# Performance work log

Hardware: AMD Instinct MI355X
Metric: run time of the kernel (lower is better)

The kernel has to match this reference:

```python
import jax, jax.numpy as jnp
import numpy as np

N = 50000
E = 800000
IN_C, OUT_C, K = 96, 16, 3
L1 = IN_C - (IN_C - OUT_C) // 3            # 70
L2 = IN_C - (2 * (IN_C - OUT_C)) // 3      # 43


def setup_inputs() -> dict:
    key = jax.random.key(0)
    ks = jax.random.split(key, 12)
    x = jax.random.normal(ks[0], (N, IN_C), dtype=jnp.float32)
    edge_index = jax.random.randint(ks[1], (2, E), 0, N, dtype=jnp.int64)

    def glorot(k, shape):
        fan_in, fan_out = shape[-2], shape[-1]
        lim = jnp.sqrt(6.0 / (fan_in + fan_out)).astype(jnp.float32)
        return jax.random.uniform(k, shape, jnp.float32, -lim, lim)

    W1 = glorot(ks[2], (K + 1, IN_C, L1)); b1 = jnp.zeros((L1,), jnp.float32)
    W2 = glorot(ks[3], (K + 1, L1, L2));   b2 = jnp.zeros((L2,), jnp.float32)
    Wmu = glorot(ks[4], (L2, OUT_C));      bmu = jnp.zeros((OUT_C,), jnp.float32)
    Wls = glorot(ks[5], (L2, OUT_C));      bls = jnp.zeros((OUT_C,), jnp.float32)
    return {"x": x, "edge_index": edge_index, "W1": W1, "b1": b1,
            "W2": W2, "b2": b2, "Wmu": Wmu, "bmu": bmu, "Wls": Wls, "bls": bls}


def _norm_no_self_loops(row, col):
    # gcn_norm, add_self_loops=False (TAGConv default)
    deg = jax.ops.segment_sum(jnp.ones((E,), jnp.float32), col, num_segments=N)
    dis = jnp.where(deg > 0, jax.lax.rsqrt(jnp.maximum(deg, 1.0)), 0.0)
    return dis[row] * dis[col]  # [E]


def _tag_conv(x, W, b, row, col, norm):
    # out = sum_k A_hat^k x W_k + b
    out = x @ W[0]
    h = x
    for k in range(1, K + 1):
        h = jax.ops.segment_sum(norm[:, None] * h[row], col, num_segments=N)
        out = out + h @ W[k]
    return out + b


def _gcn_conv(x, W, b, row, col, dis2):
    # gcn_norm with self-loops: dis2 = (deg+1)^{-1/2}
    y = x @ W
    norm = dis2[row] * dis2[col]
    agg = jax.ops.segment_sum(norm[:, None] * y[row], col, num_segments=N)
    return agg + (dis2 * dis2)[:, None] * y + b  # self-loop term + bias


def reference(x, edge_index, W1, b1, W2, b2, Wmu, bmu, Wls, bls):
    row, col = edge_index[0], edge_index[1]
    norm = _norm_no_self_loops(row, col)
    h = jax.nn.relu(_tag_conv(x, W1, b1, row, col, norm))
    h = jax.nn.relu(_tag_conv(h, W2, b2, row, col, norm))
    deg = jax.ops.segment_sum(jnp.ones((E,), jnp.float32), col, num_segments=N)
    dis2 = jax.lax.rsqrt(deg + 1.0)  # self-loops added -> deg+1 > 0
    mu = _gcn_conv(h, Wmu, bmu, row, col, dis2)
    logstd = _gcn_conv(h, Wls, bls, row, col, dis2)
    return mu, logstd
```

## Files before the change

### kernel.cpp

```cpp
#include <hip/hip_runtime.h>
#include <hip/hip_fp16.h>

static constexpr int NN  = 50000;
static constexpr int EE  = 800000;
static constexpr int CIN = 96;
static constexpr int L1C = 70, S1 = 72;
static constexpr int L2C = 43, S2P = 48;

static constexpr int IMG1U = CIN * S1 / 2;
static constexpr int IMG2U = S1 * S2P / 2;
static constexpr int IMGHU = S2P * 32 / 2;
static constexpr int NU1 = 4 * IMG1U;
static constexpr int NU2 = 4 * IMG2U;
static constexpr int TUW = NU1 + NU2 + IMGHU;
static constexpr int NBF = S1 + S2P;

static constexpr int NSLICE = 8;
static constexpr int SLICEN = NN / NSLICE;

__device__ __forceinline__ float bf_lo(unsigned int u) {
    return __uint_as_float(u << 16);
}
__device__ __forceinline__ float bf_hi(unsigned int u) {
    return __uint_as_float(u & 0xffff0000u);
}
__device__ __forceinline__ unsigned int bf_rne_bits(float f) {
    unsigned int u = __float_as_uint(f);
    return u + 0x7fffu + ((u >> 16) & 1u);
}
__device__ __forceinline__ unsigned int pack_bf(float a, float b) {
    return (bf_rne_bits(a) >> 16) | (bf_rne_bits(b) & 0xffff0000u);
}
__device__ __forceinline__ float4 unpack_bf4(uint2 q) {
    return make_float4(bf_lo(q.x), bf_hi(q.x), bf_lo(q.y), bf_hi(q.y));
}
__device__ __forceinline__ void unpack_bf8(uint4 q, float* f) {
    f[0] = bf_lo(q.x); f[1] = bf_hi(q.x); f[2] = bf_lo(q.y); f[3] = bf_hi(q.y);
    f[4] = bf_lo(q.z); f[5] = bf_hi(q.z); f[6] = bf_lo(q.w); f[7] = bf_hi(q.w);
}

__device__ __forceinline__ int rec_src(unsigned int p) { return (int)(p & 0xffffu); }
__device__ __forceinline__ float rec_w(unsigned int p) {
    return __half2float(__ushort_as_half((unsigned short)(p >> 16)));
}


__global__ void init_kernel(const float* __restrict__ W1, const float* __restrict__ b1,
                            const float* __restrict__ W2, const float* __restrict__ b2,
                            const float* __restrict__ Wmu, const float* __restrict__ Wls,
                            unsigned int* __restrict__ wB, float* __restrict__ bB,
                            int* __restrict__ deg) {
    int i = blockIdx.x * blockDim.x + threadIdx.x;
    if (i < NN) deg[i] = 0;
    if (i < TUW) {
        float v0 = 0.f, v1 = 0.f;
        if (i < NU1) {
            int img = i / IMG1U, r = i - img * IMG1U;
            int k = r / (S1 / 2), c0 = (r - k * (S1 / 2)) * 2;
            const float* Wi = W1 + (size_t)img * CIN * L1C + (size_t)k * L1C;
            if (c0 < L1C) v0 = Wi[c0];
            if (c0 + 1 < L1C) v1 = Wi[c0 + 1];
        } else if (i < NU1 + NU2) {
            int j = i - NU1;
            int img = j / IMG2U, r = j - img * IMG2U;
            int k = r / (S2P / 2), c0 = (r - k * (S2P / 2)) * 2;
            if (k < L1C) {
                const float* Wi = W2 + (size_t)img * L1C * L2C + (size_t)k * L2C;
                if (c0 < L2C) v0 = Wi[c0];
                if (c0 + 1 < L2C) v1 = Wi[c0 + 1];
            }
        } else {
            int j = i - NU1 - NU2;
            int k = j / 16, c0 = (j - k * 16) * 2;
            if (k < L2C) {
                v0 = (c0 < 16) ? Wmu[k * 16 + c0] : Wls[k * 16 + (c0 - 16)];
                int c1 = c0 + 1;
                v1 = (c1 < 16) ? Wmu[k * 16 + c1] : Wls[k * 16 + (c1 - 16)];
            }
        }
        wB[i] = pack_bf(v0, v1);
    } else if (i < TUW + NBF) {
        int j = i - TUW;
        float v = 0.f;
        if (j < S1) { if (j < L1C) v = b1[j]; }
        else { int k = j - S1; if (k < L2C) v = b2[k]; }
        bB[j] = v;
    }
}

__global__ void hist_kernel(const int* __restrict__ row, const int* __restrict__ col,
                            int* __restrict__ deg, unsigned int* __restrict__ rr, int E) {
    int e = blockIdx.x * blockDim.x + threadIdx.x;
    if (e < E) {
        int c = col[e];
        int rk = atomicAdd(&deg[c], 1);
        rr[e] = ((unsigned int)rk << 16) | (unsigned int)row[e];
    }
}

static constexpr int SB = 256;

__global__ void reduce_kernel(const int* __restrict__ deg, int* __restrict__ bsum, int n) {
    __shared__ int sd[SB];
    int i = blockIdx.x * SB + threadIdx.x;
    sd[threadIdx.x] = (i < n) ? deg[i] : 0;
    __syncthreads();
    for (int s = SB / 2; s > 0; s >>= 1) {
        if (threadIdx.x < s) sd[threadIdx.x] += sd[threadIdx.x + s];
        __syncthreads();
    }
    if (threadIdx.x == 0) bsum[blockIdx.x] = sd[0];
}

__global__ void block_scan_kernel(const int* __restrict__ deg, const int* __restrict__ bsum,
                                  int* __restrict__ off,
                                  float* __restrict__ dis, float* __restrict__ dis2,
                                  int n, int nb) {
    __shared__ int sd[SB];
    __shared__ int bofs;
    int t = threadIdx.x;
    sd[t] = (t < nb && t < (int)blockIdx.x) ? bsum[t] : 0;
    __syncthreads();
    for (int s = SB / 2; s > 0; s >>= 1) {
        if (t < s) sd[t] += sd[t + s];
        __syncthreads();
    }
    if (t == 0) bofs = sd[0];
    __syncthreads();
    int i = blockIdx.x * SB + t;
    int v = (i < n) ? deg[i] : 0;
    sd[t] = v;
    __syncthreads();
    for (int s = 1; s < SB; s <<= 1) {
        int tv = (t >= s) ? sd[t - s] : 0;
        __syncthreads();
        sd[t] += tv;
        __syncthreads();
    }
    if (i < n) {
        int e = bofs + sd[t] - v;
        off[i] = e;
        dis[i]  = (v > 0) ? rsqrtf((float)v) : 0.0f;
        dis2[i] = rsqrtf((float)v + 1.0f);
        if (i == n - 1) off[n] = e + v;
    }
}

__global__ void fill_kernel(const int* __restrict__ col, const unsigned int* __restrict__ rr,
                            const float* __restrict__ dis, const int* __restrict__ off,
                            unsigned int* __restrict__ eTag, int E) {
    int s = blockIdx.x & (NSLICE - 1);
    int nlo = s * SLICEN, nhi = nlo + SLICEN;
    int stride = (gridDim.x >> 3) * blockDim.x;
    for (int e = (blockIdx.x >> 3) * blockDim.x + threadIdx.x; e < E; e += stride) {
        int c = col[e];
        if (c >= nlo && c < nhi) {
            unsigned int u = rr[e];
            int r = (int)(u & 0xffffu);
            int pos = off[c] + (int)(u >> 16);
            unsigned short h = __half_as_ushort(__float2half(dis[r] * dis[c]));
            eTag[pos] = (unsigned int)r | ((unsigned int)h << 16);
        }
    }
}

template <int C, bool HASADD, bool RELU>
__global__ void aggw_kernel(const unsigned short* __restrict__ in, const unsigned short* addv,
                            unsigned short* out, const int* __restrict__ off,
                            const unsigned int* __restrict__ ep, int n) {
    constexpr int TPN = C / 8;
    int t = blockIdx.x * blockDim.x + threadIdx.x;
    if (t >= n * TPN) return;
    int node = t / TPN;
    int cc = (t - node * TPN) * 8;
    int beg = off[node], end = off[node + 1];
    float a0[8], a1[8];
    #pragma unroll
    for (int j = 0; j < 8; ++j) { a0[j] = 0.f; a1[j] = 0.f; }
    int e = beg;
    for (; e + 4 <= end; e += 4) {
        unsigned int p0 = ep[e], p1 = ep[e + 1], p2 = ep[e + 2], p3 = ep[e + 3];
        float w0 = rec_w(p0), w1 = rec_w(p1), w2 = rec_w(p2), w3 = rec_w(p3);
        uint4 q0 = *reinterpret_cast<const uint4*>(in + (size_t)rec_src(p0) * C + cc);
        uint4 q1 = *reinterpret_cast<const uint4*>(in + (size_t)rec_src(p1) * C + cc);
        uint4 q2 = *reinterpret_cast<const uint4*>(in + (size_t)rec_src(p2) * C + cc);
        uint4 q3 = *reinterpret_cast<const uint4*>(in + (size_t)rec_src(p3) * C + cc);
        float f[8];
        unpack_bf8(q0, f);
        #pragma unroll
        for (int j = 0; j < 8; ++j) a0[j] += w0 * f[j];
        unpack_bf8(q1, f);
        #pragma unroll
        for (int j = 0; j < 8; ++j) a1[j] += w1 * f[j];
        unpack_bf8(q2, f);
        #pragma unroll
        for (int j = 0; j < 8; ++j) a0[j] += w2 * f[j];
        unpack_bf8(q3, f);
        #pragma unroll
        for (int j = 0; j < 8; ++j) a1[j] += w3 * f[j];
    }
    for (; e < end; ++e) {
        unsigned int p = ep[e];
        float w = rec_w(p);
        uint4 q = *reinterpret_cast<const uint4*>(in + (size_t)rec_src(p) * C + cc);
        float f[8];
        unpack_bf8(q, f);
        #pragma unroll
        for (int j = 0; j < 8; ++j) a0[j] += w * f[j];
    }
    float r[8];
    #pragma unroll
    for (int j = 0; j < 8; ++j) r[j] = a0[j] + a1[j];
    if constexpr (HASADD) {
        uint4 qa = *reinterpret_cast<const uint4*>(addv + (size_t)node * C + cc);
        float f[8];
        unpack_bf8(qa, f);
        #pragma unroll
        for (int j = 0; j < 8; ++j) r[j] += f[j];
    }
    if constexpr (RELU) {
        #pragma unroll
        for (int j = 0; j < 8; ++j) r[j] = fmaxf(r[j], 0.f);
    }
    uint4 o;
    o.x = pack_bf(r[0], r[1]); o.y = pack_bf(r[2], r[3]);
    o.z = pack_bf(r[4], r[5]); o.w = pack_bf(r[6], r[7]);
    *reinterpret_cast<uint4*>(out + (size_t)node * C + cc) = o;
}

__global__ void agg_gcn_final_kernel(const unsigned short* __restrict__ yh,
                                     const int* __restrict__ off,
                                     const unsigned int* __restrict__ ep,
                                     const float* __restrict__ dis2,
                                     const float* __restrict__ bmu,
                                     const float* __restrict__ bls,
                                     float* __restrict__ outp, int n) {
    int t = blockIdx.x * blockDim.x + threadIdx.x;
    if (t >= n * 4) return;
    int node = t >> 2;
    int cc = (t & 3) * 8;
    int beg = off[node], end = off[node + 1];
    float a0[8], a1[8];
    #pragma unroll
    for (int j = 0; j < 8; ++j) { a0[j] = 0.f; a1[j] = 0.f; }
    int e = beg;
    for (; e + 2 <= end; e += 2) {
        int s0 = rec_src(ep[e]), s1 = rec_src(ep[e + 1]);
        float w0 = dis2[s0], w1 = dis2[s1];
        uint4 q0 = *reinterpret_cast<const uint4*>(yh + (size_t)s0 * 32 + cc);
        uint4 q1 = *reinterpret_cast<const uint4*>(yh + (size_t)s1 * 32 + cc);
        float f[8];
        unpack_bf8(q0, f);
        #pragma unroll
        for (int j = 0; j < 8; ++j) a0[j] += w0 * f[j];
        unpack_bf8(q1, f);
        #pragma unroll
        for (int j = 0; j < 8; ++j) a1[j] += w1 * f[j];
    }
    for (; e < end; ++e) {
        int s = rec_src(ep[e]);
        float w = dis2[s];
        uint4 q = *reinterpret_cast<const uint4*>(yh + (size_t)s * 32 + cc);
        float f[8];
        unpack_bf8(q, f);
        #pragma unroll
        for (int j = 0; j < 8; ++j) a0[j] += w * f[j];
    }
    float d = dis2[node];
    uint4 qy = *reinterpret_cast<const uint4*>(yh + (size_t)node * 32 + cc);
    float yv[8];
    unpack_bf8(qy, yv);
    const float* bp = (cc < 16) ? (bmu + cc) : (bls + (cc - 16));
    float r[8];
    #pragma unroll
    for (int j = 0; j < 8; ++j)
        r[j] = d * (a0[j] + a1[j]) + d * d * yv[j] + bp[j];
    size_t o = (cc < 16) ? ((size_t)node * 16 + cc)
                         : ((size_t)n * 16 + (size_t)node * 16 + (cc - 16));
    *reinterpret_cast<float4*>(outp + o) = make_float4(r[0], r[1], r[2], r[3]);
    *reinterpret_cast<float4*>(outp + o + 4) = make_float4(r[4], r[5], r[6], r[7]);
}

__device__ __forceinline__ void fma4(float4& a, float s, const float4& w) {
    a.x += s * w.x; a.y += s * w.y; a.z += s * w.z; a.w += s * w.w;
}

template <int KR, int PC, int NW, bool XBF, bool OBF, bool BIAS>
__global__ void mml_kernel(const void* __restrict__ Xv, const unsigned int* __restrict__ Wp,
                           const float* __restrict__ bp,
                           void* __restrict__ o0v, void* __restrict__ o1v,
                           void* __restrict__ o2v, void* __restrict__ o3v, int n) {
    constexpr int CP4 = PC / 4;
    constexpr int PCU = PC / 2;
    constexpr int WU = NW * KR * PCU;
    __shared__ __align__(16) unsigned int Wl[WU];
    __shared__ __align__(16) float bl[PC];
    {
        const uint4* s4 = reinterpret_cast<const uint4*>(Wp);
        uint4* d4 = reinterpret_cast<uint4*>(Wl);
        for (int i = threadIdx.x; i < WU / 4; i += blockDim.x) d4[i] = s4[i];
        if constexpr (BIAS)
            for (int i = threadIdx.x; i < PC; i += blockDim.x) bl[i] = bp[i];
    }
    __syncthreads();
    int idx = blockIdx.x * blockDim.x + threadIdx.x;
    if (idx >= (n >> 1) * CP4) return;
    int pair = idx / CP4;
    int c0 = (idx - pair * CP4) * 4;
    int n0 = pair * 2;
    const float* xaf = (const float*)Xv + (size_t)n0 * KR;
    const float* xbf = xaf + KR;
    const unsigned short* xah = (const unsigned short*)Xv + (size_t)n0 * KR;
    const unsigned short* xbh = xah + KR;
    const unsigned int* wc = Wl + (c0 >> 1);
    float4 acc[2][NW];
    #pragma unroll
    for (int w = 0; w < NW; ++w) {
        acc[0][w] = make_float4(0.f, 0.f, 0.f, 0.f);
        acc[1][w] = acc[0][w];
    }
    if constexpr (BIAS) {
        acc[0][0] = *reinterpret_cast<const float4*>(&bl[c0]);
        acc[1][0] = acc[0][0];
    }
    #pragma unroll 2
    for (int k4 = 0; k4 < KR / 4; ++k4) {
        float4 va, vb;
        if constexpr (XBF) {
            va = unpack_bf4(*reinterpret_cast<const uint2*>(xah + k4 * 4));
            vb = unpack_bf4(*reinterpret_cast<const uint2*>(xbh + k4 * 4));
        } else {
            va = *reinterpret_cast<const float4*>(xaf + k4 * 4);
            vb = *reinterpret_cast<const float4*>(xbf + k4 * 4);
        }
        #pragma unroll
        for (int j = 0; j < 4; ++j) {
            int k = k4 * 4 + j;
            float sa = (&va.x)[j];
            float sb = (&vb.x)[j];
            #pragma unroll
            for (int w = 0; w < NW; ++w) {
                uint2 q = *reinterpret_cast<const uint2*>(wc + (size_t)(w * KR + k) * PCU);
                float4 wv = unpack_bf4(q);
                fma4(acc[0][w], sa, wv);
                fma4(acc[1][w], sb, wv);
            }
        }
    }
    void* outs[4] = {o0v, o1v, o2v, o3v};
    #pragma unroll
    for (int w = 0; w < NW; ++w) {
        if constexpr (OBF) {
            unsigned short* o = (unsigned short*)outs[w] + (size_t)n0 * PC + c0;
            *reinterpret_cast<uint2*>(o) =
                make_uint2(pack_bf(acc[0][w].x, acc[0][w].y), pack_bf(acc[0][w].z, acc[0][w].w));
            *reinterpret_cast<uint2*>(o + PC) =
                make_uint2(pack_bf(acc[1][w].x, acc[1][w].y), pack_bf(acc[1][w].z, acc[1][w].w));
        } else {
            float* o = (float*)outs[w] + (size_t)n0 * PC + c0;
            *reinterpret_cast<float4*>(o) = acc[0][w];
            *reinterpret_cast<float4*>(o + PC) = acc[1][w];
        }
    }
}


extern "C" void kernel_launch(void* const* d_in, const int* in_sizes, int n_in,
                              void* d_out, int out_size, void* d_ws, size_t ws_size,
                              hipStream_t stream) {
    const float* x   = (const float*)d_in[0];
    const int*   ei  = (const int*)d_in[1];
    const float* W1  = (const float*)d_in[2];
    const float* b1  = (const float*)d_in[3];
    const float* W2  = (const float*)d_in[4];
    const float* b2  = (const float*)d_in[5];
    const float* Wmu = (const float*)d_in[6];
    const float* bmu = (const float*)d_in[7];
    const float* Wls = (const float*)d_in[8];
    const float* bls = (const float*)d_in[9];
    float* out = (float*)d_out;

    const int N = NN, E = EE;
    const int* row = ei;
    const int* col = ei + E;

    char* p = (char*)d_ws;
    auto alloc = [&](size_t bytes) -> char* {
        char* r = p;
        p += (bytes + 255) & ~(size_t)255;
        return r;
    };
    int*   deg    = (int*)alloc((size_t)N * 4);
    int*   off    = (int*)alloc((size_t)(N + 1) * 4);
    int*   bsum   = (int*)alloc((size_t)256 * 4);
    float* dis    = (float*)alloc((size_t)N * 4);
    float* dis2   = (float*)alloc((size_t)N * 4);
    unsigned int* wB = (unsigned int*)alloc((size_t)TUW * 4);
    float* bB     = (float*)alloc((size_t)NBF * 4);
    unsigned int* eTag = (unsigned int*)alloc((size_t)E * 4);
    unsigned int* rr   = (unsigned int*)alloc((size_t)E * 4);
    unsigned short* y0 = (unsigned short*)alloc((size_t)N * S1 * 2);
    unsigned short* y1 = (unsigned short*)alloc((size_t)N * S1 * 2);
    unsigned short* y2 = (unsigned short*)alloc((size_t)N * S1 * 2);
    unsigned short* y3 = (unsigned short*)alloc((size_t)N * S1 * 2);
    unsigned short* u0 = (unsigned short*)alloc((size_t)N * S2P * 2);
    unsigned short* u1 = (unsigned short*)alloc((size_t)N * S2P * 2);
    unsigned short* u2 = (unsigned short*)alloc((size_t)N * S2P * 2);
    unsigned short* u3 = (unsigned short*)alloc((size_t)N * S2P * 2);
    unsigned short* yh = (unsigned short*)alloc((size_t)N * 32 * 2);

    const unsigned int* W1b = wB;
    const unsigned int* W2b = wB + NU1;
    const unsigned int* Whb = wB + NU1 + NU2;
    const float* b1p = bB;
    const float* b2p = bB + S1;

    const int B = 256;
    int gE = (E + B - 1) / B;
    int nb = (N + SB - 1) / SB;

    init_kernel<<<nb, B, 0, stream>>>(W1, b1, W2, b2, Wmu, Wls, wB, bB, deg);
    hist_kernel<<<gE, B, 0, stream>>>(row, col, deg, rr, E);
    reduce_kernel<<<nb, SB, 0, stream>>>(deg, bsum, N);
    block_scan_kernel<<<nb, SB, 0, stream>>>(deg, bsum, off, dis, dis2, N, nb);
    fill_kernel<<<3200, B, 0, stream>>>(col, rr, dis, off, eTag, E);

    int gm1 = ((N / 2) * (S1 / 4) + B - 1) / B;
    int gm2 = ((N / 2) * (S2P / 4) + B - 1) / B;
    int gmh = ((N / 2) * 8 + B - 1) / B;
    int ga72 = (N * (S1 / 8) + B - 1) / B;
    int ga48 = (N * (S2P / 8) + B - 1) / B;
    int gaF  = (N * 4 + B - 1) / B;

    mml_kernel<CIN, S1, 2, false, true, true ><<<gm1, B, 0, stream>>>(
        x, W1b, b1p, y0, y1, nullptr, nullptr, N);
    mml_kernel<CIN, S1, 2, false, true, false><<<gm1, B, 0, stream>>>(
        x, W1b + 2 * IMG1U, nullptr, y2, y3, nullptr, nullptr, N);
    aggw_kernel<S1, true, false><<<ga72, B, 0, stream>>>(y3, y2, y2, off, eTag, N);
    aggw_kernel<S1, true, false><<<ga72, B, 0, stream>>>(y2, y1, y1, off, eTag, N);
    aggw_kernel<S1, true, true ><<<ga72, B, 0, stream>>>(y1, y0, y0, off, eTag, N);

    mml_kernel<S1, S2P, 4, true, true, true ><<<gm2, B, 0, stream>>>(
        y0, W2b, b2p, u0, u1, u2, u3, N);
    aggw_kernel<S2P, true, false><<<ga48, B, 0, stream>>>(u3, u2, u2, off, eTag, N);
    aggw_kernel<S2P, true, false><<<ga48, B, 0, stream>>>(u2, u1, u1, off, eTag, N);
    aggw_kernel<S2P, true, true ><<<ga48, B, 0, stream>>>(u1, u0, u0, off, eTag, N);

    mml_kernel<S2P, 32, 1, true, true, false><<<gmh, B, 0, stream>>>(
        u0, Whb, nullptr, yh, nullptr, nullptr, nullptr, N);
    agg_gcn_final_kernel<<<gaF, B, 0, stream>>>(yh, off, eTag, dis2, bmu, bls, out, N);
}
```

Baseline: 365.6 us.

## Replace scalar FMA dense layers with bf16 MFMA GEMM kernels

Replaces the per-thread FMA matmul kernels with a templated GEMM that uses 16x16x32 bf16 MFMA instructions. Weights are pre-packed into MFMA fragment layout in init_kernel, and activation tiles are staged through LDS. For the fp32 input layer, x is split into high and low bf16 parts so two MFMAs per tile keep close to fp32 accuracy. This cuts ALU work on the dense transforms in exchange for LDS staging cost and scalar 2-byte output stores.

Result: faster. 320.6 us (-12.3%).

```diff
diff --git a/kernel.cpp b/kernel.cpp
--- a/kernel.cpp
+++ b/kernel.cpp
@@ -7,16 +7,20 @@
 static constexpr int L1C = 70, S1 = 72;
 static constexpr int L2C = 43, S2P = 48;
 
-static constexpr int IMG1U = CIN * S1 / 2;
-static constexpr int IMG2U = S1 * S2P / 2;
-static constexpr int IMGHU = S2P * 32 / 2;
-static constexpr int NU1 = 4 * IMG1U;
-static constexpr int NU2 = 4 * IMG2U;
-static constexpr int TUW = NU1 + NU2 + IMGHU;
-static constexpr int NBF = S1 + S2P;
+static constexpr int NT1 = 18, KS1 = 3;
+static constexpr int NT2 = 12, KS2 = 3;
+static constexpr int NTH = 2,  KSH = 2;
+static constexpr int NU1 = NT1 * KS1 * 64 * 4;
+static constexpr int NU2 = NT2 * KS2 * 64 * 4;
+static constexpr int NUH = NTH * KSH * 64 * 4;
+static constexpr int TUW = NU1 + NU2 + NUH;
+static constexpr int NBF = 288 + 192;
 
 static constexpr int NSLICE = 8;
 static constexpr int SLICEN = NN / NSLICE;
+
+typedef short bf16x8 __attribute__((ext_vector_type(8)));
+typedef float f32x4  __attribute__((ext_vector_type(4)));
 
 __device__ __forceinline__ float bf_lo(unsigned int u) {
     return __uint_as_float(u << 16);
@@ -30,9 +34,6 @@
 }
 __device__ __forceinline__ unsigned int pack_bf(float a, float b) {
     return (bf_rne_bits(a) >> 16) | (bf_rne_bits(b) & 0xffff0000u);
-}
-__device__ __forceinline__ float4 unpack_bf4(uint2 q) {
-    return make_float4(bf_lo(q.x), bf_hi(q.x), bf_lo(q.y), bf_hi(q.y));
 }
 __device__ __forceinline__ void unpack_bf8(uint4 q, float* f) {
     f[0] = bf_lo(q.x); f[1] = bf_hi(q.x); f[2] = bf_lo(q.y); f[3] = bf_hi(q.y);
@@ -55,35 +56,47 @@
     if (i < TUW) {
         float v0 = 0.f, v1 = 0.f;
         if (i < NU1) {
-            int img = i / IMG1U, r = i - img * IMG1U;
-            int k = r / (S1 / 2), c0 = (r - k * (S1 / 2)) * 2;
-            const float* Wi = W1 + (size_t)img * CIN * L1C + (size_t)k * L1C;
-            if (c0 < L1C) v0 = Wi[c0];
-            if (c0 + 1 < L1C) v1 = Wi[c0 + 1];
+            int frag = i >> 2, j = i & 3;
+            int l = frag & 63, ts = frag >> 6;
+            int s = ts % 3, t = ts / 3;
+            int col = t * 16 + (l & 15);
+            int kb  = s * 32 + (l >> 4) * 8 + j * 2;
+            int img = col / S1, cin = col - img * S1;
+            if (cin < L1C) {
+                const float* Wp = W1 + ((size_t)img * CIN + kb) * L1C + cin;
+                v0 = Wp[0];
+                v1 = Wp[L1C];
+            }
         } else if (i < NU1 + NU2) {
-            int j = i - NU1;
-            int img = j / IMG2U, r = j - img * IMG2U;
-            int k = r / (S2P / 2), c0 = (r - k * (S2P / 2)) * 2;
-            if (k < L1C) {
-                const float* Wi = W2 + (size_t)img * L1C * L2C + (size_t)k * L2C;
-                if (c0 < L2C) v0 = Wi[c0];
-                if (c0 + 1 < L2C) v1 = Wi[c0 + 1];
+            int u = i - NU1;
+            int frag = u >> 2, j = u & 3;
+            int l = frag & 63, ts = frag >> 6;
+            int s = ts % 3, t = ts / 3;
+            int col = t * 16 + (l & 15);
+            int kb  = s * 32 + (l >> 4) * 8 + j * 2;
+            int img = col / S2P, cin = col - img * S2P;
+            if (cin < L2C) {
+                const float* Wp = W2 + ((size_t)img * L1C + kb) * L2C + cin;
+                if (kb < L1C)     v0 = Wp[0];
+                if (kb + 1 < L1C) v1 = Wp[L2C];
             }
         } else {
-            int j = i - NU1 - NU2;
-            int k = j / 16, c0 = (j - k * 16) * 2;
-            if (k < L2C) {
-                v0 = (c0 < 16) ? Wmu[k * 16 + c0] : Wls[k * 16 + (c0 - 16)];
-                int c1 = c0 + 1;
-                v1 = (c1 < 16) ? Wmu[k * 16 + c1] : Wls[k * 16 + (c1 - 16)];
-            }
+            int u = i - NU1 - NU2;
+            int frag = u >> 2, j = u & 3;
+            int l = frag & 63, ts = frag >> 6;
+            int s = ts & 1, t = ts >> 1;
+            int col = t * 16 + (l & 15);
+            int kb  = s * 32 + (l >> 4) * 8 + j * 2;
+            const float* Wsel = (col < 16) ? (Wmu + col) : (Wls + (col - 16));
+            if (kb < L2C)     v0 = Wsel[kb * 16];
+            if (kb + 1 < L2C) v1 = Wsel[(kb + 1) * 16];
         }
         wB[i] = pack_bf(v0, v1);
     } else if (i < TUW + NBF) {
         int j = i - TUW;
         float v = 0.f;
-        if (j < S1) { if (j < L1C) v = b1[j]; }
-        else { int k = j - S1; if (k < L2C) v = b2[k]; }
+        if (j < 288) { if (j < L1C) v = b1[j]; }
+        else { int c = j - 288; if (c < L2C) v = b2[c]; }
         bB[j] = v;
     }
 }
@@ -281,85 +294,106 @@
     *reinterpret_cast<float4*>(outp + o + 4) = make_float4(r[4], r[5], r[6], r[7]);
 }
 
-__device__ __forceinline__ void fma4(float4& a, float s, const float4& w) {
-    a.x += s * w.x; a.y += s * w.y; a.z += s * w.z; a.w += s * w.w;
-}
-
-template <int KR, int PC, int NW, bool XBF, bool OBF, bool BIAS>
-__global__ void mml_kernel(const void* __restrict__ Xv, const unsigned int* __restrict__ Wp,
-                           const float* __restrict__ bp,
-                           void* __restrict__ o0v, void* __restrict__ o1v,
-                           void* __restrict__ o2v, void* __restrict__ o3v, int n) {
-    constexpr int CP4 = PC / 4;
-    constexpr int PCU = PC / 2;
-    constexpr int WU = NW * KR * PCU;
-    __shared__ __align__(16) unsigned int Wl[WU];
-    __shared__ __align__(16) float bl[PC];
+template <int KS, int NT, int INS, int OIMG, bool CONV, bool BIAS>
+__launch_bounds__(256)
+__global__ void gemm_kernel(const void* __restrict__ Xv,
+                            const unsigned int* __restrict__ Wp,
+                            const float* __restrict__ bv,
+                            unsigned short* __restrict__ o0,
+                            unsigned short* __restrict__ o1,
+                            unsigned short* __restrict__ o2,
+                            unsigned short* __restrict__ o3,
+                            int n) {
+    constexpr int WFR = NT * KS * 64;
+    constexpr int XFR = KS * 256;
+    __shared__ __align__(16) unsigned int Wl[WFR * 4];
+    __shared__ __align__(16) unsigned int Xl[(CONV ? 2 : 1) * XFR * 4];
+
+    const int tid = threadIdx.x;
+    const int mb = blockIdx.x * 64;
+
     {
         const uint4* s4 = reinterpret_cast<const uint4*>(Wp);
         uint4* d4 = reinterpret_cast<uint4*>(Wl);
-        for (int i = threadIdx.x; i < WU / 4; i += blockDim.x) d4[i] = s4[i];
-        if constexpr (BIAS)
-            for (int i = threadIdx.x; i < PC; i += blockDim.x) bl[i] = bp[i];
-    }
-    __syncthreads();
-    int idx = blockIdx.x * blockDim.x + threadIdx.x;
-    if (idx >= (n >> 1) * CP4) return;
-    int pair = idx / CP4;
-    int c0 = (idx - pair * CP4) * 4;
-    int n0 = pair * 2;
-    const float* xaf = (const float*)Xv + (size_t)n0 * KR;
-    const float* xbf = xaf + KR;
-    const unsigned short* xah = (const unsigned short*)Xv + (size_t)n0 * KR;
-    const unsigned short* xbh = xah + KR;
-    const unsigned int* wc = Wl + (c0 >> 1);
-    float4 acc[2][NW];
-    #pragma unroll
-    for (int w = 0; w < NW; ++w) {
-        acc[0][w] = make_float4(0.f, 0.f, 0.f, 0.f);
-        acc[1][w] = acc[0][w];
-    }
-    if constexpr (BIAS) {
-        acc[0][0] = *reinterpret_cast<const float4*>(&bl[c0]);
-        acc[1][0] = acc[0][0];
-    }
-    #pragma unroll 2
-    for (int k4 = 0; k4 < KR / 4; ++k4) {
-        float4 va, vb;
-        if constexpr (XBF) {
-            va = unpack_bf4(*reinterpret_cast<const uint2*>(xah + k4 * 4));
-            vb = unpack_bf4(*reinterpret_cast<const uint2*>(xbh + k4 * 4));
-        } else {
-            va = *reinterpret_cast<const float4*>(xaf + k4 * 4);
-            vb = *reinterpret_cast<const float4*>(xbf + k4 * 4);
-        }
-        #pragma unroll
-        for (int j = 0; j < 4; ++j) {
-            int k = k4 * 4 + j;
-            float sa = (&va.x)[j];
-            float sb = (&vb.x)[j];
-            #pragma unroll
-            for (int w = 0; w < NW; ++w) {
-                uint2 q = *reinterpret_cast<const uint2*>(wc + (size_t)(w * KR + k) * PCU);
-                float4 wv = unpack_bf4(q);
-                fma4(acc[0][w], sa, wv);
-                fma4(acc[1][w], sb, wv);
+        for (int i = tid; i < WFR; i += 256) d4[i] = s4[i];
+    }
+    {
+        uint4* dx = reinterpret_cast<uint4*>(Xl);
+        const int l = tid & 63, w = (tid >> 6) & 3;
+        const int m = mb + w * 16 + (l & 15);
+        #pragma unroll
+        for (int s = 0; s < KS; ++s) {
+            int p = s * 256 + tid;
+            int k0 = s * 32 + (l >> 4) * 8;
+            if constexpr (CONV) {
+                bool ok = (m < n);
+                const float4* xp = reinterpret_cast<const float4*>(
+                    (const float*)Xv + (size_t)m * INS + k0);
+                float4 aa = ok ? xp[0] : make_float4(0.f, 0.f, 0.f, 0.f);
+                float4 bb = ok ? xp[1] : make_float4(0.f, 0.f, 0.f, 0.f);
+                float xv[8] = {aa.x, aa.y, aa.z, aa.w, bb.x, bb.y, bb.z, bb.w};
+                unsigned int hb[4], lb[4];
+                #pragma unroll
+                for (int j = 0; j < 4; ++j) {
+                    float a0 = xv[2 * j], a1 = xv[2 * j + 1];
+                    unsigned int h0 = bf_rne_bits(a0) & 0xffff0000u;
+                    unsigned int h1 = bf_rne_bits(a1) & 0xffff0000u;
+                    float r0 = a0 - __uint_as_float(h0);
+                    float r1 = a1 - __uint_as_float(h1);
+                    hb[j] = (h0 >> 16) | h1;
+                    lb[j] = pack_bf(r0, r1);
+                }
+                dx[p]       = make_uint4(hb[0], hb[1], hb[2], hb[3]);
+                dx[XFR + p] = make_uint4(lb[0], lb[1], lb[2], lb[3]);
+            } else {
+                uint4 v = make_uint4(0u, 0u, 0u, 0u);
+                if (m < n && k0 + 8 <= INS)
+                    v = *reinterpret_cast<const uint4*>(
+                        (const unsigned short*)Xv + (size_t)m * INS + k0);
+                dx[p] = v;
             }
         }
     }
-    void* outs[4] = {o0v, o1v, o2v, o3v};
-    #pragma unroll
-    for (int w = 0; w < NW; ++w) {
-        if constexpr (OBF) {
-            unsigned short* o = (unsigned short*)outs[w] + (size_t)n0 * PC + c0;
-            *reinterpret_cast<uint2*>(o) =
-                make_uint2(pack_bf(acc[0][w].x, acc[0][w].y), pack_bf(acc[0][w].z, acc[0][w].w));
-            *reinterpret_cast<uint2*>(o + PC) =
-                make_uint2(pack_bf(acc[1][w].x, acc[1][w].y), pack_bf(acc[1][w].z, acc[1][w].w));
-        } else {
-            float* o = (float*)outs[w] + (size_t)n0 * PC + c0;
-            *reinterpret_cast<float4*>(o) = acc[0][w];
-            *reinterpret_cast<float4*>(o + PC) = acc[1][w];
+    __syncthreads();
+
+    const int w = tid >> 6, lane = tid & 63;
+    const int ln = lane & 15, lg = lane >> 4;
+    const bf16x8* Wf = reinterpret_cast<const bf16x8*>(Wl);
+    const bf16x8* Xf = reinterpret_cast<const bf16x8*>(Xl);
+
+    f32x4 acc[NT];
+    #pragma unroll
+    for (int t = 0; t < NT; ++t) {
+        float b = 0.f;
+        if constexpr (BIAS) b = bv[t * 16 + ln];
+        acc[t] = (f32x4){b, b, b, b};
+    }
+    #pragma unroll
+    for (int s = 0; s < KS; ++s) {
+        bf16x8 ah = Xf[s * 256 + w * 64 + lane];
+        bf16x8 al;
+        if constexpr (CONV) al = Xf[XFR + s * 256 + w * 64 + lane];
+        #pragma unroll
+        for (int t = 0; t < NT; ++t) {
+            bf16x8 bw = Wf[(t * KS + s) * 64 + lane];
+            acc[t] = __builtin_amdgcn_mfma_f32_16x16x32_bf16(ah, bw, acc[t], 0, 0, 0);
+            if constexpr (CONV)
+                acc[t] = __builtin_amdgcn_mfma_f32_16x16x32_bf16(al, bw, acc[t], 0, 0, 0);
+        }
+    }
+    const int rbase = mb + w * 16 + lg * 4;
+    #pragma unroll
+    for (int t = 0; t < NT; ++t) {
+        int c = t * 16 + ln;
+        int img = c / OIMG;
+        int colin = c - img * OIMG;
+        unsigned short* ob = (img == 0) ? o0 : (img == 1) ? o1 : (img == 2) ? o2 : o3;
+        #pragma unroll
+        for (int r = 0; r < 4; ++r) {
+            int m = rbase + r;
+            if (m < n)
+                ob[(size_t)m * OIMG + colin] =
+                    (unsigned short)(bf_rne_bits(acc[t][r]) >> 16);
         }
     }
 }
@@ -412,8 +446,8 @@
     const unsigned int* W1b = wB;
     const unsigned int* W2b = wB + NU1;
     const unsigned int* Whb = wB + NU1 + NU2;
-    const float* b1p = bB;
-    const float* b2p = bB + S1;
+    const float* bv1 = bB;
+    const float* bv2 = bB + 288;
 
     const int B = 256;
     int gE = (E + B - 1) / B;
@@ -425,28 +459,26 @@
     block_scan_kernel<<<nb, SB, 0, stream>>>(deg, bsum, off, dis, dis2, N, nb);
     fill_kernel<<<3200, B, 0, stream>>>(col, rr, dis, off, eTag, E);
 
-    int gm1 = ((N / 2) * (S1 / 4) + B - 1) / B;
-    int gm2 = ((N / 2) * (S2P / 4) + B - 1) / B;
-    int gmh = ((N / 2) * 8 + B - 1) / B;
+    int gmm  = (N + 63) / 64;
     int ga72 = (N * (S1 / 8) + B - 1) / B;
     int ga48 = (N * (S2P / 8) + B - 1) / B;
     int gaF  = (N * 4 + B - 1) / B;
 
-    mml_kernel<CIN, S1, 2, false, true, true ><<<gm1, B, 0, stream>>>(
-        x, W1b, b1p, y0, y1, nullptr, nullptr, N);
-    mml_kernel<CIN, S1, 2, false, true, false><<<gm1, B, 0, stream>>>(
-        x, W1b + 2 * IMG1U, nullptr, y2, y3, nullptr, nullptr, N);
+    gemm_kernel<3, 9, CIN, S1, true, true ><<<gmm, B, 0, stream>>>(
+        x, W1b, bv1, y0, y1, y2, y3, N);
+    gemm_kernel<3, 9, CIN, S1, true, false><<<gmm, B, 0, stream>>>(
+        x, W1b + NU1 / 2, nullptr, y2, y3, y2, y3, N);
     aggw_kernel<S1, true, false><<<ga72, B, 0, stream>>>(y3, y2, y2, off, eTag, N);
     aggw_kernel<S1, true, false><<<ga72, B, 0, stream>>>(y2, y1, y1, off, eTag, N);
     aggw_kernel<S1, true, true ><<<ga72, B, 0, stream>>>(y1, y0, y0, off, eTag, N);
 
-    mml_kernel<S1, S2P, 4, true, true, true ><<<gm2, B, 0, stream>>>(
-        y0, W2b, b2p, u0, u1, u2, u3, N);
+    gemm_kernel<3, 12, S1, S2P, false, true><<<gmm, B, 0, stream>>>(
+        y0, W2b, bv2, u0, u1, u2, u3, N);
     aggw_kernel<S2P, true, false><<<ga48, B, 0, stream>>>(u3, u2, u2, off, eTag, N);
     aggw_kernel<S2P, true, false><<<ga48, B, 0, stream>>>(u2, u1, u1, off, eTag, N);
     aggw_kernel<S2P, true, true ><<<ga48, B, 0, stream>>>(u1, u0, u0, off, eTag, N);
 
-    mml_kernel<S2P, 32, 1, true, true, false><<<gmh, B, 0, stream>>>(
-        u0, Whb, nullptr, yh, nullptr, nullptr, nullptr, N);
+    gemm_kernel<2, 2, S2P, 32, false, false><<<gmm, B, 0, stream>>>(
+        u0, Whb, nullptr, yh, yh, yh, yh, N);
     agg_gcn_final_kernel<<<gaF, B, 0, stream>>>(yh, off, eTag, dis2, bmu, bls, out, N);
 }
```
